# Optimization experiments

Hardware: AMD Instinct MI355X
Metric: run time of the kernel (lower is better)

Reference implementation:

```python
import jax, jax.numpy as jnp
import numpy as np

N_WIRES = 3  # state vector of 2^3 = 8 amplitudes, kept as [B,2,2,2]


def _rx(t):
    c = jnp.cos(t / 2); s = jnp.sin(t / 2)
    return jnp.stack([jnp.stack([c + 0j, -1j * s], -1),
                      jnp.stack([-1j * s, c + 0j], -1)], -2).astype(jnp.complex64)


def _ry(t):
    c = jnp.cos(t / 2); s = jnp.sin(t / 2)
    return jnp.stack([jnp.stack([c, -s], -1),
                      jnp.stack([s, c], -1)], -2).astype(jnp.complex64)


def _rz(t):
    e = jnp.exp(-1j * t / 2).astype(jnp.complex64)
    z = jnp.zeros_like(e)
    return jnp.stack([jnp.stack([e, z], -1),
                      jnp.stack([z, jnp.conj(e)], -1)], -2)


def apply_1q(state, mat, wire):
    # state: [B,2,2,2]; mat: [2,2] (shared) or [B,2,2] (per-sample)
    s = jnp.moveaxis(state, 1 + wire, 1)
    sh = s.shape
    s = s.reshape(sh[0], 2, -1)
    m = jnp.broadcast_to(mat, (sh[0], 2, 2))
    s = jnp.einsum('bij,bjk->bik', m, s)
    return jnp.moveaxis(s.reshape(sh), 1, 1 + wire)


def apply_crx(state, t, ctrl, tgt):
    # controlled-RX: apply rx(t) to target subspace where control bit == 1
    mat = _rx(t)  # [2,2]
    s = jnp.moveaxis(state, (1 + ctrl, 1 + tgt), (1, 2))  # [B,2(ctrl),2(tgt),2]
    s1 = s[:, 1]                       # [B,2,2]
    sh = s1.shape
    s1 = jnp.einsum('ij,bjk->bik', mat, s1.reshape(sh[0], 2, -1)).reshape(sh)
    s = jnp.stack([s[:, 0], s1], 1)
    return jnp.moveaxis(s, (1, 2), (1 + ctrl, 1 + tgt))


def _quantum_forward(x, theta, W1, b1, W2, b2):
    B = x.shape[0]
    state = jnp.zeros((B, 2, 2, 2), jnp.complex64).at[:, 0, 0, 0].set(1.0)
    # GeneralEncoder: rx(x0)@w0, ry(x1)@w1, rz(x2)@w2
    state = apply_1q(state, _rx(x[:, 0]), 0)
    state = apply_1q(state, _ry(x[:, 1]), 1)
    state = apply_1q(state, _rz(x[:, 2]), 2)
    # RandomLayer(n_ops=8): fixed representative 8-op trainable sequence
    state = apply_1q(state, _rx(theta[0]), 0)
    state = apply_1q(state, _ry(theta[1]), 1)
    state = apply_1q(state, _rz(theta[2]), 2)
    state = apply_crx(state, theta[3], 0, 1)
    state = apply_1q(state, _ry(theta[4]), 2)
    state = apply_1q(state, _rx(theta[5]), 1)
    state = apply_crx(state, theta[6], 1, 2)
    state = apply_1q(state, _rz(theta[7]), 0)
    # measurement -> 8 basis-state probabilities (matches Linear(8,32) head)
    probs = (state.real ** 2 + state.imag ** 2).reshape(B, 8)
    h = jax.nn.relu(probs @ W1 + b1)
    return h @ W2 + b2


def setup_inputs() -> dict:
    key = jax.random.key(0)
    ks = jax.random.split(key, 6)
    B = 2_000_000
    x = jax.random.normal(ks[0], (B, 3), jnp.float32)
    theta = jax.random.normal(ks[1], (8,), jnp.float32)
    W1 = jax.random.normal(ks[2], (8, 32), jnp.float32) * 0.35   # ~1/sqrt(8)
    b1 = jnp.zeros((32,), jnp.float32)
    W2 = jax.random.normal(ks[3], (32, 2), jnp.float32) * 0.18   # ~1/sqrt(32)
    b2 = jnp.zeros((2,), jnp.float32)
    return {"x": x, "theta": theta, "W1": W1, "b1": b1, "W2": W2, "b2": b2}


def reference(x, theta, W1, b1, W2, b2):
    return _quantum_forward(x, theta, W1, b1, W2, b2)
```

## Files before the change

kernel.cpp:

```cpp
#include <hip/hip_runtime.h>

__global__ __launch_bounds__(64) void q_precompute(
    const float* __restrict__ theta,
    const float* __restrict__ W1,
    const float* __restrict__ b1,
    const float* __restrict__ W2,
    const float* __restrict__ b2,
    float* __restrict__ tab)
{
    __shared__ float Ure[8][8];
    __shared__ float Uim[8][8];
    const int t = threadIdx.x;

    if (t < 8) {
        float cr[8], ci[8];
        #pragma unroll
        for (int r = 0; r < 8; ++r) { cr[r] = (r == t) ? 1.f : 0.f; ci[r] = 0.f; }

        auto rxmix = [&](int a, int b, float c_, float s_) {
            float ar = cr[a], ai = ci[a], br = cr[b], bi = ci[b];
            cr[a] = c_*ar + s_*bi;   ci[a] = c_*ai - s_*br;
            cr[b] = s_*ai + c_*br;   ci[b] = -s_*ar + c_*bi;
        };
        auto rymix = [&](int a, int b, float c_, float s_) {
            float ar = cr[a], ai = ci[a], br = cr[b], bi = ci[b];
            cr[a] = c_*ar - s_*br;   ci[a] = c_*ai - s_*bi;
            cr[b] = s_*ar + c_*br;   ci[b] = s_*ai + c_*bi;
        };
        auto zmul = [&](int r, float u, float v) {
            float xr = cr[r], xi = ci[r];
            cr[r] = xr*u - xi*v;  ci[r] = xr*v + xi*u;
        };

        float c, s;
        c = cosf(theta[0]*0.5f); s = sinf(theta[0]*0.5f);
        rxmix(0,4,c,s); rxmix(1,5,c,s); rxmix(2,6,c,s); rxmix(3,7,c,s);
        c = cosf(theta[1]*0.5f); s = sinf(theta[1]*0.5f);
        rymix(0,2,c,s); rymix(1,3,c,s); rymix(4,6,c,s); rymix(5,7,c,s);
        c = cosf(theta[2]*0.5f); s = sinf(theta[2]*0.5f);
        #pragma unroll
        for (int r = 0; r < 8; ++r) zmul(r, c, (r & 1) ? s : -s);
        c = cosf(theta[3]*0.5f); s = sinf(theta[3]*0.5f);
        rxmix(4,6,c,s); rxmix(5,7,c,s);
        c = cosf(theta[4]*0.5f); s = sinf(theta[4]*0.5f);
        rymix(0,1,c,s); rymix(2,3,c,s); rymix(4,5,c,s); rymix(6,7,c,s);
        c = cosf(theta[5]*0.5f); s = sinf(theta[5]*0.5f);
        rxmix(0,2,c,s); rxmix(1,3,c,s); rxmix(4,6,c,s); rxmix(5,7,c,s);
        c = cosf(theta[6]*0.5f); s = sinf(theta[6]*0.5f);
        rxmix(2,3,c,s); rxmix(6,7,c,s);
        c = cosf(theta[7]*0.5f); s = sinf(theta[7]*0.5f);
        #pragma unroll
        for (int r = 0; r < 8; ++r) zmul(r, c, (r < 4) ? -s : s);

        #pragma unroll
        for (int r = 0; r < 8; ++r) { Ure[r][t] = cr[r]; Uim[r][t] = ci[r]; }
    }
    __syncthreads();

    if (t < 32) {
        float Wre[8][4], Wim[8][4];
        #pragma unroll
        for (int j = 0; j < 8; ++j) {
            Wre[j][0] =  Ure[j][0]; Wim[j][0] =  Uim[j][0];
            Wre[j][1] =  Ure[j][2]; Wim[j][1] =  Uim[j][2];
            Wre[j][2] =  Uim[j][4]; Wim[j][2] = -Ure[j][4];
            Wre[j][3] =  Uim[j][6]; Wim[j][3] = -Ure[j][6];
        }
        float Q[4][4];
        #pragma unroll
        for (int m = 0; m < 4; ++m)
            #pragma unroll
            for (int n = 0; n < 4; ++n) Q[m][n] = 0.f;
        for (int j = 0; j < 8; ++j) {
            float w = W1[j*32 + t];
            #pragma unroll
            for (int m = 0; m < 4; ++m)
                #pragma unroll
                for (int n = 0; n < 4; ++n)
                    Q[m][n] = fmaf(w, Wre[j][m]*Wre[j][n] + Wim[j][m]*Wim[j][n], Q[m][n]);
        }
        float R[3][3];
        R[0][0] = Q[0][0];
        R[0][1] = Q[0][1] + Q[1][0];
        R[0][2] = Q[1][1];
        R[1][0] = Q[0][2] + Q[2][0];
        R[1][1] = Q[0][3] + Q[1][2] + Q[2][1] + Q[3][0];
        R[1][2] = Q[1][3] + Q[3][1];
        R[2][0] = Q[2][2];
        R[2][1] = Q[2][3] + Q[3][2];
        R[2][2] = Q[3][3];
        float P[3][3];
        #pragma unroll
        for (int b = 0; b < 3; ++b) {
            P[0][b] = 0.5f*(R[0][b] + R[2][b]);
            P[1][b] = 0.5f*(R[0][b] - R[2][b]);
            P[2][b] = 0.5f*R[1][b];
        }
        float T[3][3];
        #pragma unroll
        for (int si = 0; si < 3; ++si) {
            T[si][0] = 0.5f*(P[si][0] + P[si][2]);
            T[si][1] = 0.5f*(P[si][0] - P[si][2]);
            T[si][2] = 0.5f*P[si][1];
        }
        float* row = tab + t*12;
        row[0] = T[0][1]; row[1] = T[0][2]; row[2] = T[1][0]; row[3] = T[2][0];
        row[4] = T[1][1]; row[5] = T[1][2]; row[6] = T[2][1]; row[7] = T[2][2];
        row[8] = b1[t] + T[0][0];
        row[9]  = W2[t*2+0];
        row[10] = W2[t*2+1];
        row[11] = 0.f;
    }
    if (t == 0) { tab[384] = b2[0]; tab[385] = b2[1]; tab[386] = 0.f; tab[387] = 0.f; }
}

__global__ __launch_bounds__(256) void q_main(
    const float* __restrict__ x,
    const float* __restrict__ tab,
    float* __restrict__ out,
    int B)
{
    __shared__ float4 lt[97];
    const int lid = threadIdx.x;
    if (lid < 97) lt[lid] = ((const float4*)tab)[lid];
    __syncthreads();

    const int t = blockIdx.x * 256 + lid;
    const int base = t * 4;
    if (base >= B) return;

    const float* ltf = (const float*)lt;
    const float b2a = ltf[384], b2b = ltf[385];

    if (base + 4 <= B) {
        const float4* X4 = (const float4*)x;
        float4 xa = X4[t*3+0], xb = X4[t*3+1], xc = X4[t*3+2];
        float a0[4] = {xa.x, xa.w, xb.z, xc.y};
        float a1[4] = {xa.y, xb.x, xb.w, xc.z};

        float C0[4], S0[4], C1[4], S1[4], P00[4], P01[4], P10[4], P11[4];
        #pragma unroll
        for (int k = 0; k < 4; ++k) {
            __sincosf(a0[k], &S0[k], &C0[k]);
            __sincosf(a1[k], &S1[k], &C1[k]);
            P00[k] = C0[k]*C1[k]; P01[k] = C0[k]*S1[k];
            P10[k] = S0[k]*C1[k]; P11[k] = S0[k]*S1[k];
        }
        float acc0[4] = {b2a, b2a, b2a, b2a};
        float acc1[4] = {b2b, b2b, b2b, b2b};

        #pragma unroll 2
        for (int l = 0; l < 32; ++l) {
            float4 cA = lt[l*3+0];
            float4 cB = lt[l*3+1];
            float4 cC = lt[l*3+2];
            #pragma unroll
            for (int k = 0; k < 4; ++k) {
                float h = cC.x;
                h = fmaf(cA.x, C1[k],  h);
                h = fmaf(cA.y, S1[k],  h);
                h = fmaf(cA.z, C0[k],  h);
                h = fmaf(cA.w, S0[k],  h);
                h = fmaf(cB.x, P00[k], h);
                h = fmaf(cB.y, P01[k], h);
                h = fmaf(cB.z, P10[k], h);
                h = fmaf(cB.w, P11[k], h);
                h = fmaxf(h, 0.f);
                acc0[k] = fmaf(h, cC.y, acc0[k]);
                acc1[k] = fmaf(h, cC.z, acc1[k]);
            }
        }
        float4* O4 = (float4*)out;
        O4[t*2+0] = make_float4(acc0[0], acc1[0], acc0[1], acc1[1]);
        O4[t*2+1] = make_float4(acc0[2], acc1[2], acc0[3], acc1[3]);
    } else {
        for (int e = base; e < B; ++e) {
            float s0, c0, s1, c1;
            __sincosf(x[e*3+0], &s0, &c0);
            __sincosf(x[e*3+1], &s1, &c1);
            float p00 = c0*c1, p01 = c0*s1, p10 = s0*c1, p11 = s0*s1;
            float A0 = b2a, A1 = b2b;
            for (int l = 0; l < 32; ++l) {
                const float* row = ltf + l*12;
                float h = row[8];
                h = fmaf(row[0], c1,  h);
                h = fmaf(row[1], s1,  h);
                h = fmaf(row[2], c0,  h);
                h = fmaf(row[3], s0,  h);
                h = fmaf(row[4], p00, h);
                h = fmaf(row[5], p01, h);
                h = fmaf(row[6], p10, h);
                h = fmaf(row[7], p11, h);
                h = fmaxf(h, 0.f);
                A0 = fmaf(h, row[9],  A0);
                A1 = fmaf(h, row[10], A1);
            }
            out[e*2+0] = A0;
            out[e*2+1] = A1;
        }
    }
}

extern "C" void kernel_launch(void* const* d_in, const int* in_sizes, int n_in,
                              void* d_out, int out_size, void* d_ws, size_t ws_size,
                              hipStream_t stream) {
    const float* x     = (const float*)d_in[0];
    const float* theta = (const float*)d_in[1];
    const float* W1    = (const float*)d_in[2];
    const float* b1    = (const float*)d_in[3];
    const float* W2    = (const float*)d_in[4];
    const float* b2    = (const float*)d_in[5];
    float* out = (float*)d_out;
    float* tab = (float*)d_ws;

    const int B = in_sizes[0] / 3;

    q_precompute<<<1, 64, 0, stream>>>(theta, W1, b1, W2, b2, tab);

    const int nT = (B + 3) / 4;
    const int blocks = (nT + 255) / 256;
    q_main<<<blocks, 256, 0, stream>>>(x, tab, out, B);
}
```

Measured before the change: 114.3 us.

## Fuse table precompute into main kernel and process eight samples per thread

Removes the separate single-block precompute launch: every block now rebuilds the 8x8 unitary and the 32-row coefficient table in shared memory, and the x loads are issued before that work so their latency overlaps it. Each thread now handles eight samples instead of four, which halves the grid and amortizes the shared-memory table reads over more FMAs. The costs are redundant per-block precompute (sincos, a small matrix build, global reads of W1/W2), higher register pressure under launch_bounds(256,4), and fast __sincosf replacing cosf/sinf for theta.

```diff
diff --git a/kernel.cpp b/kernel.cpp
--- a/kernel.cpp
+++ b/kernel.cpp
@@ -1,21 +1,35 @@
 #include <hip/hip_runtime.h>
 
-__global__ __launch_bounds__(64) void q_precompute(
+__global__ __launch_bounds__(256, 4) void q_fused(
+    const float* __restrict__ x,
     const float* __restrict__ theta,
     const float* __restrict__ W1,
     const float* __restrict__ b1,
     const float* __restrict__ W2,
     const float* __restrict__ b2,
-    float* __restrict__ tab)
+    float* __restrict__ out,
+    int B)
 {
     __shared__ float Ure[8][8];
     __shared__ float Uim[8][8];
-    const int t = threadIdx.x;
-
-    if (t < 8) {
+    __shared__ float4 lt4[98];
+
+    const int lid  = threadIdx.x;
+    const int t    = blockIdx.x * 256 + lid;
+    const int base = t * 8;
+    const bool full = (base + 8 <= B);
+
+    float4 xa[6];
+    if (full) {
+        const float4* X4 = (const float4*)x;
+        #pragma unroll
+        for (int i = 0; i < 6; ++i) xa[i] = X4[t*6 + i];
+    }
+
+    if (lid < 8) {
         float cr[8], ci[8];
         #pragma unroll
-        for (int r = 0; r < 8; ++r) { cr[r] = (r == t) ? 1.f : 0.f; ci[r] = 0.f; }
+        for (int r = 0; r < 8; ++r) { cr[r] = (r == lid) ? 1.f : 0.f; ci[r] = 0.f; }
 
         auto rxmix = [&](int a, int b, float c_, float s_) {
             float ar = cr[a], ai = ci[a], br = cr[b], bi = ci[b];
@@ -33,31 +47,31 @@
         };
 
         float c, s;
-        c = cosf(theta[0]*0.5f); s = sinf(theta[0]*0.5f);
+        __sincosf(theta[0]*0.5f, &s, &c);
         rxmix(0,4,c,s); rxmix(1,5,c,s); rxmix(2,6,c,s); rxmix(3,7,c,s);
-        c = cosf(theta[1]*0.5f); s = sinf(theta[1]*0.5f);
+        __sincosf(theta[1]*0.5f, &s, &c);
         rymix(0,2,c,s); rymix(1,3,c,s); rymix(4,6,c,s); rymix(5,7,c,s);
-        c = cosf(theta[2]*0.5f); s = sinf(theta[2]*0.5f);
+        __sincosf(theta[2]*0.5f, &s, &c);
         #pragma unroll
         for (int r = 0; r < 8; ++r) zmul(r, c, (r & 1) ? s : -s);
-        c = cosf(theta[3]*0.5f); s = sinf(theta[3]*0.5f);
+        __sincosf(theta[3]*0.5f, &s, &c);
         rxmix(4,6,c,s); rxmix(5,7,c,s);
-        c = cosf(theta[4]*0.5f); s = sinf(theta[4]*0.5f);
+        __sincosf(theta[4]*0.5f, &s, &c);
         rymix(0,1,c,s); rymix(2,3,c,s); rymix(4,5,c,s); rymix(6,7,c,s);
-        c = cosf(theta[5]*0.5f); s = sinf(theta[5]*0.5f);
+        __sincosf(theta[5]*0.5f, &s, &c);
         rxmix(0,2,c,s); rxmix(1,3,c,s); rxmix(4,6,c,s); rxmix(5,7,c,s);
-        c = cosf(theta[6]*0.5f); s = sinf(theta[6]*0.5f);
+        __sincosf(theta[6]*0.5f, &s, &c);
         rxmix(2,3,c,s); rxmix(6,7,c,s);
-        c = cosf(theta[7]*0.5f); s = sinf(theta[7]*0.5f);
+        __sincosf(theta[7]*0.5f, &s, &c);
         #pragma unroll
         for (int r = 0; r < 8; ++r) zmul(r, c, (r < 4) ? -s : s);
 
         #pragma unroll
-        for (int r = 0; r < 8; ++r) { Ure[r][t] = cr[r]; Uim[r][t] = ci[r]; }
+        for (int r = 0; r < 8; ++r) { Ure[r][lid] = cr[r]; Uim[r][lid] = ci[r]; }
     }
     __syncthreads();
 
-    if (t < 32) {
+    if (lid < 32) {
         float Wre[8][4], Wim[8][4];
         #pragma unroll
         for (int j = 0; j < 8; ++j) {
@@ -71,8 +85,9 @@
         for (int m = 0; m < 4; ++m)
             #pragma unroll
             for (int n = 0; n < 4; ++n) Q[m][n] = 0.f;
+        #pragma unroll
         for (int j = 0; j < 8; ++j) {
-            float w = W1[j*32 + t];
+            float w = W1[j*32 + lid];
             #pragma unroll
             for (int m = 0; m < 4; ++m)
                 #pragma unroll
@@ -103,82 +118,69 @@
             T[si][1] = 0.5f*(P[si][0] - P[si][2]);
             T[si][2] = 0.5f*P[si][1];
         }
-        float* row = tab + t*12;
+        float* row = ((float*)lt4) + lid*12;
         row[0] = T[0][1]; row[1] = T[0][2]; row[2] = T[1][0]; row[3] = T[2][0];
         row[4] = T[1][1]; row[5] = T[1][2]; row[6] = T[2][1]; row[7] = T[2][2];
-        row[8] = b1[t] + T[0][0];
-        row[9]  = W2[t*2+0];
-        row[10] = W2[t*2+1];
+        row[8] = b1[lid] + T[0][0];
+        row[9]  = W2[lid*2+0];
+        row[10] = W2[lid*2+1];
         row[11] = 0.f;
     }
-    if (t == 0) { tab[384] = b2[0]; tab[385] = b2[1]; tab[386] = 0.f; tab[387] = 0.f; }
-}
-
-__global__ __launch_bounds__(256) void q_main(
-    const float* __restrict__ x,
-    const float* __restrict__ tab,
-    float* __restrict__ out,
-    int B)
-{
-    __shared__ float4 lt[97];
-    const int lid = threadIdx.x;
-    if (lid < 97) lt[lid] = ((const float4*)tab)[lid];
+    if (lid == 0) {
+        float* f = (float*)lt4;
+        f[384] = b2[0]; f[385] = b2[1]; f[386] = 0.f; f[387] = 0.f;
+        f[388] = 0.f;   f[389] = 0.f;   f[390] = 0.f; f[391] = 0.f;
+    }
     __syncthreads();
 
-    const int t = blockIdx.x * 256 + lid;
-    const int base = t * 4;
-    if (base >= B) return;
-
-    const float* ltf = (const float*)lt;
+    const float* ltf = (const float*)lt4;
     const float b2a = ltf[384], b2b = ltf[385];
 
-    if (base + 4 <= B) {
-        const float4* X4 = (const float4*)x;
-        float4 xa = X4[t*3+0], xb = X4[t*3+1], xc = X4[t*3+2];
-        float a0[4] = {xa.x, xa.w, xb.z, xc.y};
-        float a1[4] = {xa.y, xb.x, xb.w, xc.z};
-
-        float C0[4], S0[4], C1[4], S1[4], P00[4], P01[4], P10[4], P11[4];
-        #pragma unroll
-        for (int k = 0; k < 4; ++k) {
-            __sincosf(a0[k], &S0[k], &C0[k]);
-            __sincosf(a1[k], &S1[k], &C1[k]);
-            P00[k] = C0[k]*C1[k]; P01[k] = C0[k]*S1[k];
-            P10[k] = S0[k]*C1[k]; P11[k] = S0[k]*S1[k];
-        }
-        float acc0[4] = {b2a, b2a, b2a, b2a};
-        float acc1[4] = {b2b, b2b, b2b, b2b};
-
-        #pragma unroll 2
+    if (full) {
+        const float* xf = (const float*)xa;
+        float C0[8], S0[8], C1[8], S1[8], Pcc[8], Pcs[8], Psc[8], Pss[8];
+        #pragma unroll
+        for (int k = 0; k < 8; ++k) {
+            __sincosf(xf[3*k+0], &S0[k], &C0[k]);
+            __sincosf(xf[3*k+1], &S1[k], &C1[k]);
+            Pcc[k] = C0[k]*C1[k]; Pcs[k] = C0[k]*S1[k];
+            Psc[k] = S0[k]*C1[k]; Pss[k] = S0[k]*S1[k];
+        }
+        float acc0[8], acc1[8];
+        #pragma unroll
+        for (int k = 0; k < 8; ++k) { acc0[k] = b2a; acc1[k] = b2b; }
+
+        #pragma unroll 1
         for (int l = 0; l < 32; ++l) {
-            float4 cA = lt[l*3+0];
-            float4 cB = lt[l*3+1];
-            float4 cC = lt[l*3+2];
+            float4 cA = lt4[l*3+0];
+            float4 cB = lt4[l*3+1];
+            float4 cC = lt4[l*3+2];
             #pragma unroll
-            for (int k = 0; k < 4; ++k) {
+            for (int k = 0; k < 8; ++k) {
                 float h = cC.x;
                 h = fmaf(cA.x, C1[k],  h);
                 h = fmaf(cA.y, S1[k],  h);
                 h = fmaf(cA.z, C0[k],  h);
                 h = fmaf(cA.w, S0[k],  h);
-                h = fmaf(cB.x, P00[k], h);
-                h = fmaf(cB.y, P01[k], h);
-                h = fmaf(cB.z, P10[k], h);
-                h = fmaf(cB.w, P11[k], h);
+                h = fmaf(cB.x, Pcc[k], h);
+                h = fmaf(cB.y, Pcs[k], h);
+                h = fmaf(cB.z, Psc[k], h);
+                h = fmaf(cB.w, Pss[k], h);
                 h = fmaxf(h, 0.f);
                 acc0[k] = fmaf(h, cC.y, acc0[k]);
                 acc1[k] = fmaf(h, cC.z, acc1[k]);
             }
         }
         float4* O4 = (float4*)out;
-        O4[t*2+0] = make_float4(acc0[0], acc1[0], acc0[1], acc1[1]);
-        O4[t*2+1] = make_float4(acc0[2], acc1[2], acc0[3], acc1[3]);
-    } else {
+        #pragma unroll
+        for (int k = 0; k < 4; ++k)
+            O4[t*4+k] = make_float4(acc0[2*k], acc1[2*k], acc0[2*k+1], acc1[2*k+1]);
+    } else if (base < B) {
         for (int e = base; e < B; ++e) {
             float s0, c0, s1, c1;
             __sincosf(x[e*3+0], &s0, &c0);
             __sincosf(x[e*3+1], &s1, &c1);
-            float p00 = c0*c1, p01 = c0*s1, p10 = s0*c1, p11 = s0*s1;
+            float pcc = c0*c1, pcs = c0*s1, psc = s0*c1, pss = s0*s1;
             float A0 = b2a, A1 = b2b;
             for (int l = 0; l < 32; ++l) {
                 const float* row = ltf + l*12;
@@ -187,10 +189,10 @@
                 h = fmaf(row[1], s1,  h);
                 h = fmaf(row[2], c0,  h);
                 h = fmaf(row[3], s0,  h);
-                h = fmaf(row[4], p00, h);
-                h = fmaf(row[5], p01, h);
-                h = fmaf(row[6], p10, h);
-                h = fmaf(row[7], p11, h);
+                h = fmaf(row[4], pcc, h);
+                h = fmaf(row[5], pcs, h);
+                h = fmaf(row[6], psc, h);
+                h = fmaf(row[7], pss, h);
                 h = fmaxf(h, 0.f);
                 A0 = fmaf(h, row[9],  A0);
                 A1 = fmaf(h, row[10], A1);
@@ -211,13 +213,9 @@
     const float* W2    = (const float*)d_in[4];
     const float* b2    = (const float*)d_in[5];
     float* out = (float*)d_out;
-    float* tab = (float*)d_ws;
 
     const int B = in_sizes[0] / 3;
-
-    q_precompute<<<1, 64, 0, stream>>>(theta, W1, b1, W2, b2, tab);
-
-    const int nT = (B + 3) / 4;
+    const int nT = (B + 7) / 8;
     const int blocks = (nT + 255) / 256;
-    q_main<<<blocks, 256, 0, stream>>>(x, tab, out, B);
+    q_fused<<<blocks, 256, 0, stream>>>(x, theta, W1, b1, W2, b2, out, B);
 }
```

Result: faster. 104.1 us (-8.9%).
